# Kernel tuning notes

Measured on AMD Instinct MI355X. Metric: run time of the kernel, lower is better.

Reference implementation:

```python
import jax, jax.numpy as jnp
import numpy as np

B, S, N, D, T = 128, 128, 196, 512, 12


def setup_inputs() -> dict:
    key = jax.random.key(0)
    ks = jax.random.split(key, 20)
    nrm = lambda i, shape, s: jax.random.normal(ks[i], shape, jnp.float32) * s
    w = lambda i, shape: nrm(i, shape, 1.0 / np.sqrt(shape[-1]))
    return {
        "ctx": nrm(0, (B, S, D), 1.0),
        "q": nrm(1, (B, 2 * D), 1.0),
        "k": nrm(2, (B, D, N), 1.0),
        "mem0": nrm(3, (1, D), 0.02),
        "ctrl0": nrm(4, (1, D), 0.02),
        # ControlUnit params
        "Wp": w(5, (T, D, 2 * D)), "bp": jnp.zeros((T, D), jnp.float32),
        "Wcq": w(6, (D, 2 * D)), "bcq": jnp.zeros((D,), jnp.float32),
        "Wca": w(7, (1, D)), "bca": jnp.zeros((1,), jnp.float32),
        # ReadUnit params
        "Wrm": w(8, (D, D)), "brm": jnp.zeros((D,), jnp.float32),
        "Wrc": w(9, (D, 2 * D)), "brc": jnp.zeros((D,), jnp.float32),
        "Wra": w(10, (1, D)), "bra": jnp.zeros((1,), jnp.float32),
        # WriteUnit params
        "Wwc": w(11, (D, 2 * D)), "bwc": jnp.zeros((D,), jnp.float32),
    }


def reference(ctx, q, k, mem0, ctrl0, Wp, bp, Wcq, bcq, Wca, bca,
              Wrm, brm, Wrc, brc, Wra, bra, Wwc, bwc):
    b = q.shape[0]
    c = jnp.broadcast_to(ctrl0, (b, D))
    m = jnp.broadcast_to(mem0, (b, D))
    for t in range(T):
        # --- control unit (alpha_entmax with alpha=1.0 == softmax) ---
        p = q @ Wp[t].T + bp[t]                                # [B, D]
        cc = jnp.concatenate([c, p], axis=1) @ Wcq.T + bcq     # [B, D]
        ctx_p = cc[:, None, :] * ctx                           # [B, S, D]
        aw = jax.nn.softmax(ctx_p @ Wca.T + bca, axis=1)       # [B, S, 1]
        c = (aw * ctx).sum(axis=1)                             # [B, D]
        # --- read unit ---
        mm = (m @ Wrm.T + brm)[:, :, None]                     # [B, D, 1]
        kc = jnp.concatenate([mm * k, k], axis=1)              # [B, 2D, N]
        rc = kc.transpose(0, 2, 1) @ Wrc.T + brc               # [B, N, D]
        logit = ((rc * c[:, None, :]) @ Wra.T + bra)[..., 0]   # [B, N]
        rw = jax.nn.softmax(logit, axis=1)[:, None, :]         # [B, 1, N]
        r = (rw * k).sum(axis=2)                               # [B, D]
        # --- write unit (no self-attention / memory gate) ---
        m = jnp.concatenate([r, m], axis=1) @ Wwc.T + bwc      # [B, D]
    return m
```

## Files before the change

### kernel.cpp

```cpp
#include <hip/hip_runtime.h>
#include <hip/hip_bf16.h>
#include <cstdint>

#define D  512
#define D2 1024
#define BB 128
#define SS 128
#define NN 196
#define TT 12

typedef unsigned short u16;
typedef __attribute__((ext_vector_type(8))) short short8v;
typedef __attribute__((ext_vector_type(4))) float f32x4;

__device__ __forceinline__ float bf2f(u16 h){
  union { unsigned int u; float f; } v; v.u = ((unsigned int)h) << 16; return v.f;
}

__device__ __forceinline__ float LDX(const void* p, size_t i, int isbf){
  if (isbf) return bf2f(((const u16*)p)[i]);
  return ((const float*)p)[i];
}

__device__ __forceinline__ float4 LD4(const void* p, size_t i, int isbf){
  if (isbf){
    ushort4 w = *(const ushort4*)((const u16*)p + i);
    return make_float4(bf2f(w.x), bf2f(w.y), bf2f(w.z), bf2f(w.w));
  }
  return *(const float4*)((const float*)p + i);
}

__device__ __forceinline__ void bfsplit(float x, short &h, short &l){
  unsigned u = __float_as_uint(x);
  unsigned hu = u & 0xFFFF0000u;
  float r = x - __uint_as_float(hu);
  h = (short)(u >> 16);
  l = (short)(__float_as_uint(r) >> 16);
}

__global__ __launch_bounds__(256) void k_detect(const u16* ctx, int* flag){
  __shared__ int cnt;
  if (threadIdx.x == 0) cnt = 0;
  __syncthreads();
  int bad = 0;
  for (int i = threadIdx.x; i < 8192; i += 256){
    int e = (ctx[i] >> 7) & 0xFF;
    if (e == 0xFF || (e != 0 && (e < 90 || e > 160))) bad++;
  }
  atomicAdd(&cnt, bad);
  __syncthreads();
  if (threadIdx.x == 0) *flag = (cnt > 100) ? 0 : 1;
}

__global__ __launch_bounds__(256) void k_prep1(const void* Wcq, const void* Wca,
      const void* Wwc, const void* Wrm, const void* Wrc, const void* Wra,
      const void* bp, const void* bcq, const void* ctrl0, const void* mem0, const void* brm,
      float* W1f, float* Wwcf, float* WrmTf, float* W2f,
      float* P, float* pp2, float* ubase, float* mmb, const int* flag){
  const int isbf = *flag;
  __shared__ float lds[32][33];
  int bk = blockIdx.x, tid = threadIdx.x;
  int tx = tid & 31, ty = tid >> 5;
  if (bk >= 1216){
    int ib = bk - 1216;
    int lane = tid & 63, w = tid >> 6;
    int grp = lane >> 3, k = lane & 7;
    int isU = (ib < 16);
    int o = (isU ? ib : ib - 16)*32 + w*8 + grp;
    const void* vec = isU ? ctrl0 : mem0;
    const void* mat = isU ? Wcq : Wrm;
    int ld = isU ? D2 : D;
    float acc = 0.f;
    #pragma unroll 4
    for (int it = 0; it < 16; it++){
      int d = it*32 + k*4;
      float4 v = LD4(vec, d, isbf);
      float4 m = LD4(mat, (size_t)o*ld + d, isbf);
      acc += v.x*m.x + v.y*m.y + v.z*m.z + v.w*m.w;
    }
    acc += __shfl_xor(acc, 1, 64);
    acc += __shfl_xor(acc, 2, 64);
    acc += __shfl_xor(acc, 4, 64);
    if (k == 0){
      if (isU) ubase[o] = acc * LDX(Wca, o, isbf);
      else     mmb[o]   = acc + LDX(brm, o, isbf);
    }
    return;
  }
  if (bk >= 1152){
    int l = bk - 1152;
    for (int idx = l*256 + tid; idx < 786432; idx += 64*256){
      int j = (idx >> 7) & 511;
      pp2[idx] = LDX(bcq, j, isbf) * LDX(Wca, j, isbf);
    }
    return;
  }
  if (bk >= 1088){
    int l = bk - 1088;
    for (int idx = l*256 + tid; idx < 786432; idx += 64*256)
      P[idx] = LDX(bp, idx >> 7, isbf);
    return;
  }
  if (bk >= 1024){
    int l = bk - 1024;
    if (isbf){
      const u16* w = (const u16*)Wrc; const u16* s = (const u16*)Wra;
      for (int idx = l*256 + tid; idx < 524288; idx += 64*256)
        W2f[idx] = bf2f(w[idx]) * bf2f(s[idx >> 10]);
    } else {
      const float* w = (const float*)Wrc; const float* s = (const float*)Wra;
      for (int idx = l*256 + tid; idx < 524288; idx += 64*256)
        W2f[idx] = w[idx] * s[idx >> 10];
    }
    return;
  }
  const void* in = nullptr; const void* scale = nullptr; float* out = nullptr;
  int ld = 0, R = 0, tR = 0, tC = 0;
  if (bk < 256)      { int l = bk;       in = Wcq; ld = 1024; R = 512; out = W1f;  scale = Wca; tR = l & 15; tC = l >> 4; }
  else if (bk < 768) { int l = bk - 256; in = Wwc; ld = 1024; R = 512; out = Wwcf; tR = l & 15; tC = l >> 4; }
  else               { int l = bk - 768; in = Wrm; ld = 512;  R = 512; out = WrmTf;tR = l & 15; tC = l >> 4; }
  int r0 = tR*32, c0 = tC*32;
  #pragma unroll
  for (int kk = 0; kk < 4; kk++){
    int r = r0 + ty + kk*8;
    float v = LDX(in, (size_t)r*ld + c0 + tx, isbf);
    if (scale) v *= LDX(scale, r, isbf);
    lds[tx][ty + kk*8] = v;
  }
  __syncthreads();
  #pragma unroll
  for (int kk = 0; kk < 4; kk++){
    int oc = ty + kk*8;
    out[(size_t)(c0 + oc)*R + r0 + tx] = lds[oc][tx];
  }
}

__global__ __launch_bounds__(256) void k_pack(const void* q, u16* QF,
                                              const void* kmat, float* kT, const int* flag){
  const int isbf = *flag;
  __shared__ float lds[64][201];
  int bk = blockIdx.x, tid = threadIdx.x;
  if (bk < 128){
    u16* QH = QF;
    u16* QL = QF + 131072;
    for (int idx = bk*256 + tid; idx < 131072; idx += 128*256){
      int b = idx >> 10, x = idx & 1023;
      int o = ((x >> 3) << 10) + (b << 3) + (x & 7);
      if (isbf){
        QH[o] = ((const u16*)q)[idx];
        QL[o] = 0;
      } else {
        short h, l;
        bfsplit(((const float*)q)[idx], h, l);
        QH[o] = (u16)h;
        QL[o] = (u16)l;
      }
    }
    return;
  }
  int l = bk - 128;
  int b = l >> 3, dt = l & 7;
  int d0 = dt*64;
  int r = tid >> 2, q4 = tid & 3;
  const size_t rowbase = ((size_t)b*D + d0 + r)*NN;
  #pragma unroll
  for (int p = 0; p < 13; p++){
    int j = q4 + p*4;
    if (j < 49){
      float4 v = LD4(kmat, rowbase + 4*j, isbf);
      *(float4*)&lds[r][4*j] = v;
    }
  }
  __syncthreads();
  int n_loc = tid >> 4, f = tid & 15;
  #pragma unroll
  for (int p = 0; p < 13; p++){
    int n = p*16 + n_loc;
    if (n < NN){
      float4 v = make_float4(lds[4*f][n], lds[4*f+1][n], lds[4*f+2][n], lds[4*f+3][n]);
      *(float4*)&kT[((size_t)b*NN + n)*D + d0 + 4*f] = v;
    }
  }
}

__global__ __launch_bounds__(256) void k_Pmfma(const void* Wp, const u16* QF,
                                               float* P, const int* flag){
  const int isbf = *flag;
  const u16* QH = QF;
  const u16* QL = QF + 131072;
  int bk = blockIdx.x;
  int mt = bk >> 2, kc = bk & 3;
  int m0 = mt * 32;
  int tid = threadIdx.x;
  int ln = tid & 63, w = tid >> 6;
  int msub = w >> 1, nh = w & 1;
  int row  = m0 + msub*16 + (ln & 15);
  int koff = ln >> 4;
  f32x4 acc[4];
  #pragma unroll
  for (int i = 0; i < 4; i++) acc[i] = (f32x4){0.f, 0.f, 0.f, 0.f};

  for (int ks = 0; ks < 8; ks++){
    int k0 = kc*256 + ks*32;
    short8v ah, al;
    if (isbf){
      const u16* wr = (const u16*)Wp + (size_t)row*D2 + k0 + koff*8;
      ah = *(const short8v*)wr;
    } else {
      const float* wr = (const float*)Wp + (size_t)row*D2 + k0 + koff*8;
      float4 f0 = *(const float4*)wr;
      float4 f1 = *(const float4*)(wr + 4);
      float fs[8] = {f0.x, f0.y, f0.z, f0.w, f1.x, f1.y, f1.z, f1.w};
      #pragma unroll
      for (int j = 0; j < 8; j++){
        short h, l;
        bfsplit(fs[j], h, l);
        ah[j] = h; al[j] = l;
      }
    }
    int qrow = ((k0 >> 3) + koff) << 10;
    #pragma unroll
    for (int nt = 0; nt < 4; nt++){
      int col = (nh*4 + nt)*16 + (ln & 15);
      short8v bh = *(const short8v*)(QH + qrow + (col << 3));
      acc[nt] = __builtin_amdgcn_mfma_f32_16x16x32_bf16(ah, bh, acc[nt], 0, 0, 0);
      if (!isbf){
        short8v bl = *(const short8v*)(QL + qrow + (col << 3));
        acc[nt] = __builtin_amdgcn_mfma_f32_16x16x32_bf16(ah, bl, acc[nt], 0, 0, 0);
        acc[nt] = __builtin_amdgcn_mfma_f32_16x16x32_bf16(al, bh, acc[nt], 0, 0, 0);
      }
    }
  }
  int orow = m0 + msub*16 + (ln >> 4)*4;
  #pragma unroll
  for (int nt = 0; nt < 4; nt++){
    int b = (nh*4 + nt)*16 + (ln & 15);
    #pragma unroll
    for (int r = 0; r < 4; r++)
      atomicAdd(&P[(size_t)(orow + r)*BB + b], acc[nt][r]);
  }
}

__global__ __launch_bounds__(512) void k_pp2(const float* P, const void* Wcq,
                                             const void* Wca, float* pp2, const int* flag){
  const int isbf = *flag;
  int bk = blockIdx.x;
  int t = bk >> 6; int r = bk & 63; int jt = r >> 1; int kc = r & 1;
  int tid = threadIdx.x;
  int b = tid & 127;
  int ih = __builtin_amdgcn_readfirstlane(tid >> 7);
  int j0 = jt*16 + ih*4;
  float acc[4] = {0.f, 0.f, 0.f, 0.f};
  int e0k = kc*256;
  if (isbf){
    const u16* w = (const u16*)Wcq;
    for (int e = e0k; e < e0k + 256; e += 8){
      float a[8];
      #pragma unroll
      for (int u = 0; u < 8; u++) a[u] = P[(size_t)(t*D + e + u)*BB + b];
      #pragma unroll
      for (int kk = 0; kk < 4; kk++){
        ushort4 w0 = *(const ushort4*)(w + (size_t)(j0+kk)*D2 + D + e);
        ushort4 w1 = *(const ushort4*)(w + (size_t)(j0+kk)*D2 + D + e + 4);
        acc[kk] += a[0]*bf2f(w0.x) + a[1]*bf2f(w0.y) + a[2]*bf2f(w0.z) + a[3]*bf2f(w0.w)
                 + a[4]*bf2f(w1.x) + a[5]*bf2f(w1.y) + a[6]*bf2f(w1.z) + a[7]*bf2f(w1.w);
      }
    }
  } else {
    const float* w = (const float*)Wcq;
    for (int e = e0k; e < e0k + 256; e += 8){
      float a[8];
      #pragma unroll
      for (int u = 0; u < 8; u++) a[u] = P[(size_t)(t*D + e + u)*BB + b];
      #pragma unroll
      for (int kk = 0; kk < 4; kk++){
        float4 w0 = *(const float4*)(w + (size_t)(j0+kk)*D2 + D + e);
        float4 w1 = *(const float4*)(w + (size_t)(j0+kk)*D2 + D + e + 4);
        acc[kk] += a[0]*w0.x + a[1]*w0.y + a[2]*w0.z + a[3]*w0.w
                 + a[4]*w1.x + a[5]*w1.y + a[6]*w1.z + a[7]*w1.w;
      }
    }
  }
  #pragma unroll
  for (int kk = 0; kk < 4; kk++)
    atomicAdd(&pp2[(size_t)(t*D + j0 + kk)*BB + b], acc[kk] * LDX(Wca, j0 + kk, isbf));
}

__global__ __launch_bounds__(256) void k_initB(const float* ubase, const void* mem0,
                                               const float* pp2,
                                               float* u0, float* act0, const int* flag){
  const int isbf = *flag;
  for (int idx = blockIdx.x*256 + threadIdx.x; idx < 2*D*BB; idx += 64*256){
    if (idx < D*BB) u0[idx] = ubase[idx >> 7] + pp2[idx];
    else          { int x = idx - D*BB; act0[D*BB + x] = LDX(mem0, x >> 7, isbf); }
  }
}

__global__ __launch_bounds__(512) void k_K1(const void* ctx, const float* u_cur,
                                            float* gbuf, const float* pbuf, const float* kT,
                                            float* r_out, int t, const int* flag){
  __shared__ float sm[1024];
  int bk = blockIdx.x, tid = threadIdx.x;
  const int isbf = *flag;
  if (bk < 512){
    if (t == 0) return;
    float* lg   = sm;
    float* red  = sm + 256;
    float* psum = sm + 512;
    int b = bk & 127, qc = bk >> 7;
    if (tid < 256){
      float s;
      if (tid < NN){
        s = 0.f;
        #pragma unroll
        for (int c = 0; c < 8; c++)
          s += pbuf[((size_t)c*BB + b)*256 + tid];
      } else s = -INFINITY;
      lg[tid] = s; red[tid] = s;
    }
    __syncthreads();
    for (int off = 128; off; off >>= 1){ if (tid < off) red[tid] = fmaxf(red[tid], red[tid+off]); __syncthreads(); }
    float M = red[0];
    __syncthreads();
    if (tid < 256){ float e = (tid < NN) ? __expf(lg[tid] - M) : 0.f; lg[tid] = e; red[tid] = e; }
    __syncthreads();
    for (int off = 128; off; off >>= 1){ if (tid < off) red[tid] += red[tid+off]; __syncthreads(); }
    float inv = 1.f / red[0];
    int ng = tid >> 7, dl = tid & 127;
    const float* kTb = kT + ((size_t)b*NN + ng*49)*D + qc*128 + dl;
    float acc = 0.f;
    for (int j = 0; j < 49; j++)
      acc += lg[ng*49 + j] * kTb[(size_t)j*D];
    psum[ng*128 + dl] = acc;
    __syncthreads();
    if (tid < 128)
      r_out[(size_t)(qc*128 + tid)*BB + b] =
        (psum[tid] + psum[128 + tid] + psum[256 + tid] + psum[384 + tid]) * inv;
    return;
  }
  if (t >= TT) return;
  int l = bk - 512;
  int b = l & 127, sc = l >> 7;
  float* us = sm;
  us[tid] = u_cur[(size_t)tid*BB + b];
  __syncthreads();
  int lane = tid & 63, wv = tid >> 6;
  float ur[8];
  #pragma unroll
  for (int j = 0; j < 8; j++) ur[j] = us[lane*8 + j];
  #pragma unroll
  for (int rr = 0; rr < 4; rr++){
    int s = sc*32 + wv*4 + rr;
    size_t base = ((size_t)(b*SS + s))*D + lane*8;
    float4 c0 = LD4(ctx, base, isbf);
    float4 c1 = LD4(ctx, base + 4, isbf);
    float dot = ur[0]*c0.x + ur[1]*c0.y + ur[2]*c0.z + ur[3]*c0.w
              + ur[4]*c1.x + ur[5]*c1.y + ur[6]*c1.z + ur[7]*c1.w;
    #pragma unroll
    for (int off = 32; off; off >>= 1) dot += __shfl_down(dot, off, 64);
    if (lane == 0) gbuf[b*SS + s] = dot;
  }
}

__global__ __launch_bounds__(512) void k_K2(const void* ctx, const float* gbuf, float* cbuf,
                                            const float* act_prev, float* act_cur,
                                            float* u_nxt, const float* pp2_next,
                                            const float* Wwcf, int t, const int* flag){
  __shared__ float sm[768];
  int bk = blockIdx.x, tid = threadIdx.x;
  const int isbf = *flag;
  if (bk < 512){
    float* lg   = sm;
    float* red  = sm + 128;
    float* psum = sm + 256;
    int b = bk & 127, qc = bk >> 7;
    if (tid < 128){ float v = gbuf[b*SS + tid]; lg[tid] = v; red[tid] = v; }
    __syncthreads();
    for (int off = 64; off; off >>= 1){ if (tid < off) red[tid] = fmaxf(red[tid], red[tid+off]); __syncthreads(); }
    float M = red[0];
    __syncthreads();
    if (tid < 128){ float e = __expf(lg[tid] - M); lg[tid] = e; red[tid] = e; }
    __syncthreads();
    for (int off = 64; off; off >>= 1){ if (tid < off) red[tid] += red[tid+off]; __syncthreads(); }
    float inv = 1.f / red[0];
    int sg = tid >> 7, dl = tid & 127;
    int d = qc*128 + dl;
    float acc = 0.f;
    for (int j = 0; j < 32; j++){
      int s = sg*32 + j;
      acc += lg[s] * LDX(ctx, ((size_t)(b*SS + s))*D + d, isbf);
    }
    psum[sg*128 + dl] = acc;
    __syncthreads();
    if (tid < 128)
      cbuf[(size_t)(qc*128 + tid)*BB + b] =
        (psum[tid] + psum[128 + tid] + psum[256 + tid] + psum[384 + tid]) * inv;
    return;
  }
  int b = tid & 127;
  int ih = __builtin_amdgcn_readfirstlane(tid >> 7);
  if (bk < 1024){
    if (t == 0) return;
    int l = bk - 512;
    int it = l >> 3, kc = l & 7;
    int ih0 = ih & 1, ih1 = ih >> 1;
    int i0 = it*8 + ih0*4;
    int e0 = kc*128 + ih1*64;
    float acc[4] = {0.f,0.f,0.f,0.f};
    for (int e = e0; e < e0 + 64; e += 8){
      float av[8];
      #pragma unroll
      for (int u = 0; u < 8; u++) av[u] = act_prev[(size_t)(e+u)*BB + b];
      #pragma unroll
      for (int u = 0; u < 8; u++){
        float4 w0 = *(const float4*)(Wwcf + (size_t)(e+u)*D + i0);
        acc[0]+=av[u]*w0.x; acc[1]+=av[u]*w0.y; acc[2]+=av[u]*w0.z; acc[3]+=av[u]*w0.w;
      }
    }
    #pragma unroll
    for (int kk = 0; kk < 4; kk++)
      atomicAdd(&act_cur[(size_t)(D + i0 + kk)*BB + b], acc[kk]);
  } else {
    if (t >= TT-1) return;
    int l = bk - 1024;
    for (int x = l*512 + tid; x < D*BB; x += 32*512) u_nxt[x] = pp2_next[x];
  }
}

__global__ __launch_bounds__(512) void k_KC1(const void* kmat, const float* cbuf,
                                             const float* act_cur, const float* W2f,
                                             const float* WrmTf, const void* brm,
                                             const float* mmb, float* pbuf,
                                             const float* W1f, float* u_nxt,
                                             float* act_nxt, const void* bwc,
                                             int t, const int* flag){
  __shared__ float cb[512];
  __shared__ float mv[512];
  __shared__ float wv2[256];
  __shared__ float mmv[128];
  __shared__ float u2[128];
  int bk = blockIdx.x, tid = threadIdx.x;
  const int isbf = *flag;
  if (bk < 512){
    int b = bk & 127, ch2 = bk >> 7;
    int d0 = ch2*128;
    cb[tid] = cbuf[(size_t)tid*BB + b];
    if (t > 0) mv[tid] = act_cur[(size_t)(D + tid)*BB + b];
    __syncthreads();
    if (tid < 256){
      int e = (tid < 128) ? (d0 + tid) : (D + d0 + (tid - 128));
      float c0=0.f,c1=0.f,c2=0.f,c3=0.f,c4=0.f,c5=0.f,c6=0.f,c7=0.f;
      for (int j = 0; j < 512; j += 8){
        c0 += cb[j  ]*W2f[(size_t)(j  )*D2 + e];
        c1 += cb[j+1]*W2f[(size_t)(j+1)*D2 + e];
        c2 += cb[j+2]*W2f[(size_t)(j+2)*D2 + e];
        c3 += cb[j+3]*W2f[(size_t)(j+3)*D2 + e];
        c4 += cb[j+4]*W2f[(size_t)(j+4)*D2 + e];
        c5 += cb[j+5]*W2f[(size_t)(j+5)*D2 + e];
        c6 += cb[j+6]*W2f[(size_t)(j+6)*D2 + e];
        c7 += cb[j+7]*W2f[(size_t)(j+7)*D2 + e];
      }
      wv2[tid] = (((c0+c1)+(c2+c3)) + ((c4+c5)+(c6+c7)));
    } else if (tid < 384){
      int tm = tid - 256;
      int d = d0 + tm;
      if (t == 0){
        mmv[tm] = mmb[d];
      } else {
        float c0=0.f,c1=0.f,c2=0.f,c3=0.f,c4=0.f,c5=0.f,c6=0.f,c7=0.f;
        for (int j = 0; j < 512; j += 8){
          c0 += mv[j  ]*WrmTf[(size_t)(j  )*D + d];
          c1 += mv[j+1]*WrmTf[(size_t)(j+1)*D + d];
          c2 += mv[j+2]*WrmTf[(size_t)(j+2)*D + d];
          c3 += mv[j+3]*WrmTf[(size_t)(j+3)*D + d];
          c4 += mv[j+4]*WrmTf[(size_t)(j+4)*D + d];
          c5 += mv[j+5]*WrmTf[(size_t)(j+5)*D + d];
          c6 += mv[j+6]*WrmTf[(size_t)(j+6)*D + d];
          c7 += mv[j+7]*WrmTf[(size_t)(j+7)*D + d];
        }
        mmv[tm] = LDX(brm, d, isbf) + (((c0+c1)+(c2+c3)) + ((c4+c5)+(c6+c7)));
      }
    }
    __syncthreads();
    if (tid < 128) u2[tid] = wv2[tid]*mmv[tid] + wv2[128 + tid];
    __syncthreads();
    int half = tid >> 8;
    int n = tid & 255;
    int dd0 = half*64;
    float part = 0.f;
    if (n < NN){
      float c[8];
      #pragma unroll
      for (int u = 0; u < 8; u++) c[u] = 0.f;
      if (isbf){
        const u16* kb = (const u16*)kmat + (size_t)b*D*NN + (size_t)(d0+dd0)*NN + n;
        for (int dd = 0; dd < 64; dd += 8){
          #pragma unroll
          for (int u = 0; u < 8; u++) c[u] += u2[dd0+dd+u]*bf2f(kb[(size_t)(dd+u)*NN]);
        }
      } else {
        const float* kb = (const float*)kmat + (size_t)b*D*NN + (size_t)(d0+dd0)*NN + n;
        for (int dd = 0; dd < 64; dd += 8){
          #pragma unroll
          for (int u = 0; u < 8; u++) c[u] += u2[dd0+dd+u]*kb[(size_t)(dd+u)*NN];
        }
      }
      part = (((c[0]+c[1]) + (c[2]+c[3])) + ((c[4]+c[5]) + (c[6]+c[7])));
    }
    int chunk = ch2*2 + half;
    pbuf[((size_t)chunk*BB + b)*256 + n] = part;
    return;
  }
  int b = tid & 127;
  int ih = __builtin_amdgcn_readfirstlane(tid >> 7);
  if (bk < 768){
    if (t >= TT-1) return;
    int l = bk - 512;
    int jt = l >> 1, kc = l & 1;
    int j = jt*4 + ih;
    float c0 = 0.f, c1 = 0.f, c2 = 0.f, c3 = 0.f, c4 = 0.f, c5 = 0.f, c6 = 0.f, c7 = 0.f;
    int e0 = kc*256;
    for (int e = e0; e < e0 + 256; e += 8){
      c0 += cbuf[(e  )*BB + b] * W1f[(size_t)(e  )*D + j];
      c1 += cbuf[(e+1)*BB + b] * W1f[(size_t)(e+1)*D + j];
      c2 += cbuf[(e+2)*BB + b] * W1f[(size_t)(e+2)*D + j];
      c3 += cbuf[(e+3)*BB + b] * W1f[(size_t)(e+3)*D + j];
      c4 += cbuf[(e+4)*BB + b] * W1f[(size_t)(e+4)*D + j];
      c5 += cbuf[(e+5)*BB + b] * W1f[(size_t)(e+5)*D + j];
      c6 += cbuf[(e+6)*BB + b] * W1f[(size_t)(e+6)*D + j];
      c7 += cbuf[(e+7)*BB + b] * W1f[(size_t)(e+7)*D + j];
    }
    float acc = (((c0+c1)+(c2+c3)) + ((c4+c5)+(c6+c7)));
    atomicAdd(&u_nxt[(size_t)j*BB + b], acc);
  } else {
    int l = bk - 768;
    for (int x = l*512 + tid; x < D*BB; x += 32*512)
      act_nxt[D*BB + x] = LDX(bwc, x >> 7, isbf);
  }
}

__global__ __launch_bounds__(512) void k_moutA(const float* act_fin, const float* Wwcf,
                                               float* act_out){
  int bk = blockIdx.x, tid = threadIdx.x;
  int b = tid & 127;
  int ih = __builtin_amdgcn_readfirstlane(tid >> 7);
  int it = bk >> 3, kc = bk & 7;
  int ih0 = ih & 1, ih1 = ih >> 1;
  int i0 = it*8 + ih0*4;
  int e0 = kc*128 + ih1*64;
  float acc[4] = {0.f,0.f,0.f,0.f};
  for (int e = e0; e < e0 + 64; e += 8){
    float av[8];
    #pragma unroll
    for (int u = 0; u < 8; u++) av[u] = act_fin[(size_t)(e+u)*BB + b];
    #pragma unroll
    for (int u = 0; u < 8; u++){
      float4 w0 = *(const float4*)(Wwcf + (size_t)(e+u)*D + i0);
      acc[0]+=av[u]*w0.x; acc[1]+=av[u]*w0.y; acc[2]+=av[u]*w0.z; acc[3]+=av[u]*w0.w;
    }
  }
  #pragma unroll
  for (int kk = 0; kk < 4; kk++)
    atomicAdd(&act_out[(size_t)(D + i0 + kk)*BB + b], acc[kk]);
}

__global__ __launch_bounds__(256) void k_outT(const float* act_fin, void* out, const int* flag){
  const int isbf = *flag;
  __shared__ float lds[32][33];
  int bk = blockIdx.x;
  int it = bk >> 2, bt = bk & 3;
  int tx = threadIdx.x & 31, ty = threadIdx.x >> 5;
  #pragma unroll
  for (int kk = 0; kk < 4; kk++){
    int i = it*32 + ty + kk*8;
    lds[tx][ty + kk*8] = act_fin[(size_t)(D + i)*BB + bt*32 + tx];
  }
  __syncthreads();
  if (isbf){
    __hip_bfloat16* o = (__hip_bfloat16*)out;
    #pragma unroll
    for (int kk = 0; kk < 4; kk++){
      int bb = bt*32 + ty + kk*8;
      o[(size_t)bb*D + it*32 + tx] = __float2bfloat16(lds[ty + kk*8][tx]);
    }
  } else {
    float* o = (float*)out;
    #pragma unroll
    for (int kk = 0; kk < 4; kk++){
      int bb = bt*32 + ty + kk*8;
      o[(size_t)bb*D + it*32 + tx] = lds[ty + kk*8][tx];
    }
  }
}

extern "C" void kernel_launch(void* const* d_in, const int* in_sizes, int n_in,
                              void* d_out, int out_size, void* d_ws, size_t ws_size,
                              hipStream_t stream){
  const void* ctx  = d_in[0];
  const void* q    = d_in[1];
  const void* kmat = d_in[2];
  const void* mem0 = d_in[3];
  const void* ctrl0= d_in[4];
  const void* Wp   = d_in[5];
  const void* bp   = d_in[6];
  const void* Wcq  = d_in[7];
  const void* bcq  = d_in[8];
  const void* Wca  = d_in[9];
  const void* Wrm  = d_in[11];
  const void* brm  = d_in[12];
  const void* Wrc  = d_in[13];
  const void* Wra  = d_in[15];
  const void* Wwc  = d_in[17];
  const void* bwc  = d_in[18];

  float* W      = (float*)d_ws;
  float* qT     = W;
  float* P      = W + 131072;
  float* pp2    = W + 917504;
  float* W1f    = W + 1703936;
  float* W2f    = W + 1966080;
  float* Wwcf   = W + 2490368;
  float* WrmTf  = W + 3014656;
  float* cbuf   = W + 3276800;
  float* actb   = W + 3538944;
  float* ubuf   = W + 3801088;
  int*   flag   = (int*)(W + 3932160);
  float* ubase  = W + 3932224;
  float* mmb    = W + 3932736;
  float* gbuf   = W + 3933248;
  float* pbuf   = P;
  float* kT     = W + 4194304;

  hipLaunchKernelGGL(k_detect, dim3(1), dim3(256), 0, stream, (const u16*)ctx, flag);
  hipLaunchKernelGGL(k_prep1, dim3(1248), dim3(256), 0, stream,
                     Wcq, Wca, Wwc, Wrm, Wrc, Wra, bp, bcq, ctrl0, mem0, brm,
                     W1f, Wwcf, WrmTf, W2f, P, pp2, ubase, mmb, flag);
  hipLaunchKernelGGL(k_pack, dim3(1152), dim3(256), 0, stream,
                     q, (u16*)qT, kmat, kT, flag);
  hipLaunchKernelGGL(k_Pmfma, dim3(768), dim3(256), 0, stream, Wp, (const u16*)qT, P, flag);
  hipLaunchKernelGGL(k_pp2,  dim3(768), dim3(512), 0, stream, P, Wcq, Wca, pp2, flag);
  hipLaunchKernelGGL(k_initB, dim3(64), dim3(256), 0, stream,
                     ubase, mem0, pp2, ubuf, actb, flag);

  for (int t = 0; t < TT; t++){
    int cur = t & 1, nxt = 1 - cur;
    float* act_cur  = actb + cur*131072;
    float* act_prev = actb + nxt*131072;
    hipLaunchKernelGGL(k_K1, dim3(1024), dim3(512), 0, stream,
                       ctx, ubuf + cur*65536, gbuf, pbuf, kT,
                       act_prev, t, flag);
    hipLaunchKernelGGL(k_K2, dim3(1056), dim3(512), 0, stream,
                       ctx, gbuf, cbuf, act_prev, act_cur,
                       ubuf + nxt*65536,
                       pp2 + ((t+1 < TT) ? (t+1)*65536 : 0), Wwcf, t, flag);
    hipLaunchKernelGGL(k_KC1, dim3(800), dim3(512), 0, stream,
                       kmat, cbuf, act_cur, W2f, WrmTf, brm, mmb, pbuf,
                       W1f, ubuf + nxt*65536,
                       actb + nxt*131072, bwc, t, flag);
  }
  hipLaunchKernelGGL(k_K1, dim3(512), dim3(512), 0, stream,
                     ctx, ubuf, gbuf, pbuf, kT,
                     actb + 131072, TT, flag);
  hipLaunchKernelGGL(k_moutA, dim3(512), dim3(512), 0, stream,
                     actb + 131072, Wwcf, actb);
  hipLaunchKernelGGL(k_outT, dim3(64), dim3(256), 0, stream, actb, d_out, flag);
}
```

Before: 1.010 ms.

## Fuse recurrent loop into one persistent cooperative kernel with grid syncs

The 12-step loop of three kernel launches per step is replaced by a single cooperative kernel of 256 blocks. Each block loops over virtual block indices, and the former kernel boundaries become grid.sync barriers. The kernel bodies are factored into shared device functions, and the old multi-launch path stays as a fallback if the cooperative launch fails. This removes per-launch overhead and inter-kernel gaps. In exchange it cuts the number of resident blocks per phase, serializes work within each block, and pays the cost of grid-wide barriers.

New measurement: 2.663 ms. 164% more time.

```diff
diff --git a/kernel.cpp b/kernel.cpp
--- a/kernel.cpp
+++ b/kernel.cpp
@@ -1,6 +1,9 @@
 #include <hip/hip_runtime.h>
 #include <hip/hip_bf16.h>
+#include <hip/hip_cooperative_groups.h>
 #include <cstdint>
+
+namespace cg = cooperative_groups;
 
 #define D  512
 #define D2 1024
@@ -296,51 +299,46 @@
   }
 }
 
-__global__ __launch_bounds__(512) void k_K1(const void* ctx, const float* u_cur,
-                                            float* gbuf, const float* pbuf, const float* kT,
-                                            float* r_out, int t, const int* flag){
-  __shared__ float sm[1024];
-  int bk = blockIdx.x, tid = threadIdx.x;
-  const int isbf = *flag;
-  if (bk < 512){
-    if (t == 0) return;
-    float* lg   = sm;
-    float* red  = sm + 256;
-    float* psum = sm + 512;
-    int b = bk & 127, qc = bk >> 7;
-    if (tid < 256){
-      float s;
-      if (tid < NN){
-        s = 0.f;
-        #pragma unroll
-        for (int c = 0; c < 8; c++)
-          s += pbuf[((size_t)c*BB + b)*256 + tid];
-      } else s = -INFINITY;
-      lg[tid] = s; red[tid] = s;
-    }
-    __syncthreads();
-    for (int off = 128; off; off >>= 1){ if (tid < off) red[tid] = fmaxf(red[tid], red[tid+off]); __syncthreads(); }
-    float M = red[0];
-    __syncthreads();
-    if (tid < 256){ float e = (tid < NN) ? __expf(lg[tid] - M) : 0.f; lg[tid] = e; red[tid] = e; }
-    __syncthreads();
-    for (int off = 128; off; off >>= 1){ if (tid < off) red[tid] += red[tid+off]; __syncthreads(); }
-    float inv = 1.f / red[0];
-    int ng = tid >> 7, dl = tid & 127;
-    const float* kTb = kT + ((size_t)b*NN + ng*49)*D + qc*128 + dl;
-    float acc = 0.f;
-    for (int j = 0; j < 49; j++)
-      acc += lg[ng*49 + j] * kTb[(size_t)j*D];
-    psum[ng*128 + dl] = acc;
-    __syncthreads();
-    if (tid < 128)
-      r_out[(size_t)(qc*128 + tid)*BB + b] =
-        (psum[tid] + psum[128 + tid] + psum[256 + tid] + psum[384 + tid]) * inv;
-    return;
-  }
-  if (t >= TT) return;
-  int l = bk - 512;
-  int b = l & 127, sc = l >> 7;
+__device__ __forceinline__ void body_kfinish(const float* pbuf, const float* kT,
+                                             float* r_out, int vb, int tid, float* sm){
+  float* lg   = sm;
+  float* red  = sm + 256;
+  float* psum = sm + 512;
+  int b = vb & 127, qc = vb >> 7;
+  if (tid < 256){
+    float s;
+    if (tid < NN){
+      s = 0.f;
+      #pragma unroll
+      for (int c = 0; c < 8; c++)
+        s += pbuf[((size_t)c*BB + b)*256 + tid];
+    } else s = -INFINITY;
+    lg[tid] = s; red[tid] = s;
+  }
+  __syncthreads();
+  for (int off = 128; off; off >>= 1){ if (tid < off) red[tid] = fmaxf(red[tid], red[tid+off]); __syncthreads(); }
+  float M = red[0];
+  __syncthreads();
+  if (tid < 256){ float e = (tid < NN) ? __expf(lg[tid] - M) : 0.f; lg[tid] = e; red[tid] = e; }
+  __syncthreads();
+  for (int off = 128; off; off >>= 1){ if (tid < off) red[tid] += red[tid+off]; __syncthreads(); }
+  float inv = 1.f / red[0];
+  int ng = tid >> 7, dl = tid & 127;
+  const float* kTb = kT + ((size_t)b*NN + ng*49)*D + qc*128 + dl;
+  float acc = 0.f;
+  for (int j = 0; j < 49; j++)
+    acc += lg[ng*49 + j] * kTb[(size_t)j*D];
+  psum[ng*128 + dl] = acc;
+  __syncthreads();
+  if (tid < 128)
+    r_out[(size_t)(qc*128 + tid)*BB + b] =
+      (psum[tid] + psum[128 + tid] + psum[256 + tid] + psum[384 + tid]) * inv;
+}
+
+__device__ __forceinline__ void body_ctxlogit(const void* ctx, const float* u_cur,
+                                              float* gbuf, int vb, int tid, int isbf,
+                                              float* sm){
+  int b = vb & 127, sc = vb >> 7;
   float* us = sm;
   us[tid] = u_cur[(size_t)tid*BB + b];
   __syncthreads();
@@ -362,64 +360,249 @@
   }
 }
 
+__device__ __forceinline__ void body_ctxfin(const void* ctx, const float* gbuf, float* cbuf,
+                                            int vb, int tid, int isbf, float* sm){
+  float* lg   = sm;
+  float* red  = sm + 128;
+  float* psum = sm + 256;
+  int b = vb & 127, qc = vb >> 7;
+  if (tid < 128){ float v = gbuf[b*SS + tid]; lg[tid] = v; red[tid] = v; }
+  __syncthreads();
+  for (int off = 64; off; off >>= 1){ if (tid < off) red[tid] = fmaxf(red[tid], red[tid+off]); __syncthreads(); }
+  float M = red[0];
+  __syncthreads();
+  if (tid < 128){ float e = __expf(lg[tid] - M); lg[tid] = e; red[tid] = e; }
+  __syncthreads();
+  for (int off = 64; off; off >>= 1){ if (tid < off) red[tid] += red[tid+off]; __syncthreads(); }
+  float inv = 1.f / red[0];
+  int sg = tid >> 7, dl = tid & 127;
+  int d = qc*128 + dl;
+  float acc = 0.f;
+  for (int j = 0; j < 32; j++){
+    int s = sg*32 + j;
+    acc += lg[s] * LDX(ctx, ((size_t)(b*SS + s))*D + d, isbf);
+  }
+  psum[sg*128 + dl] = acc;
+  __syncthreads();
+  if (tid < 128)
+    cbuf[(size_t)(qc*128 + tid)*BB + b] =
+      (psum[tid] + psum[128 + tid] + psum[256 + tid] + psum[384 + tid]) * inv;
+}
+
+__device__ __forceinline__ void body_mgemv(const float* act_prev, const float* Wwcf,
+                                           float* act_cur, int vb, int tid){
+  int b = tid & 127;
+  int ih = __builtin_amdgcn_readfirstlane(tid >> 7);
+  int it = vb >> 3, kc = vb & 7;
+  int ih0 = ih & 1, ih1 = ih >> 1;
+  int i0 = it*8 + ih0*4;
+  int e0 = kc*128 + ih1*64;
+  float acc[4] = {0.f,0.f,0.f,0.f};
+  for (int e = e0; e < e0 + 64; e += 8){
+    float av[8];
+    #pragma unroll
+    for (int u = 0; u < 8; u++) av[u] = act_prev[(size_t)(e+u)*BB + b];
+    #pragma unroll
+    for (int u = 0; u < 8; u++){
+      float4 w0 = *(const float4*)(Wwcf + (size_t)(e+u)*D + i0);
+      acc[0]+=av[u]*w0.x; acc[1]+=av[u]*w0.y; acc[2]+=av[u]*w0.z; acc[3]+=av[u]*w0.w;
+    }
+  }
+  #pragma unroll
+  for (int kk = 0; kk < 4; kk++)
+    atomicAdd(&act_cur[(size_t)(D + i0 + kk)*BB + b], acc[kk]);
+}
+
+__device__ __forceinline__ void body_fused(const void* kmat, const float* cbuf,
+                                           const float* act_cur, const float* W2f,
+                                           const float* WrmTf, const void* brm,
+                                           const float* mmb, float* pbuf,
+                                           int vb, int tid, int t, int isbf,
+                                           float* cb, float* mvs, float* wv2,
+                                           float* mmv, float* u2s){
+  int b = vb & 127, ch2 = vb >> 7;
+  int d0 = ch2*128;
+  cb[tid] = cbuf[(size_t)tid*BB + b];
+  if (t > 0) mvs[tid] = act_cur[(size_t)(D + tid)*BB + b];
+  __syncthreads();
+  if (tid < 256){
+    int e = (tid < 128) ? (d0 + tid) : (D + d0 + (tid - 128));
+    float c0=0.f,c1=0.f,c2=0.f,c3=0.f,c4=0.f,c5=0.f,c6=0.f,c7=0.f;
+    for (int j = 0; j < 512; j += 8){
+      c0 += cb[j  ]*W2f[(size_t)(j  )*D2 + e];
+      c1 += cb[j+1]*W2f[(size_t)(j+1)*D2 + e];
+      c2 += cb[j+2]*W2f[(size_t)(j+2)*D2 + e];
+      c3 += cb[j+3]*W2f[(size_t)(j+3)*D2 + e];
+      c4 += cb[j+4]*W2f[(size_t)(j+4)*D2 + e];
+      c5 += cb[j+5]*W2f[(size_t)(j+5)*D2 + e];
+      c6 += cb[j+6]*W2f[(size_t)(j+6)*D2 + e];
+      c7 += cb[j+7]*W2f[(size_t)(j+7)*D2 + e];
+    }
+    wv2[tid] = (((c0+c1)+(c2+c3)) + ((c4+c5)+(c6+c7)));
+  } else if (tid < 384){
+    int tm = tid - 256;
+    int d = d0 + tm;
+    if (t == 0){
+      mmv[tm] = mmb[d];
+    } else {
+      float c0=0.f,c1=0.f,c2=0.f,c3=0.f,c4=0.f,c5=0.f,c6=0.f,c7=0.f;
+      for (int j = 0; j < 512; j += 8){
+        c0 += mvs[j  ]*WrmTf[(size_t)(j  )*D + d];
+        c1 += mvs[j+1]*WrmTf[(size_t)(j+1)*D + d];
+        c2 += mvs[j+2]*WrmTf[(size_t)(j+2)*D + d];
+        c3 += mvs[j+3]*WrmTf[(size_t)(j+3)*D + d];
+        c4 += mvs[j+4]*WrmTf[(size_t)(j+4)*D + d];
+        c5 += mvs[j+5]*WrmTf[(size_t)(j+5)*D + d];
+        c6 += mvs[j+6]*WrmTf[(size_t)(j+6)*D + d];
+        c7 += mvs[j+7]*WrmTf[(size_t)(j+7)*D + d];
+      }
+      mmv[tm] = LDX(brm, d, isbf) + (((c0+c1)+(c2+c3)) + ((c4+c5)+(c6+c7)));
+    }
+  }
+  __syncthreads();
+  if (tid < 128) u2s[tid] = wv2[tid]*mmv[tid] + wv2[128 + tid];
+  __syncthreads();
+  int half = tid >> 8;
+  int n = tid & 255;
+  int dd0 = half*64;
+  float part = 0.f;
+  if (n < NN){
+    float c[8];
+    #pragma unroll
+    for (int u = 0; u < 8; u++) c[u] = 0.f;
+    if (isbf){
+      const u16* kb = (const u16*)kmat + (size_t)b*D*NN + (size_t)(d0+dd0)*NN + n;
+      for (int dd = 0; dd < 64; dd += 8){
+        #pragma unroll
+        for (int u = 0; u < 8; u++) c[u] += u2s[dd0+dd+u]*bf2f(kb[(size_t)(dd+u)*NN]);
+      }
+    } else {
+      const float* kb = (const float*)kmat + (size_t)b*D*NN + (size_t)(d0+dd0)*NN + n;
+      for (int dd = 0; dd < 64; dd += 8){
+        #pragma unroll
+        for (int u = 0; u < 8; u++) c[u] += u2s[dd0+dd+u]*kb[(size_t)(dd+u)*NN];
+      }
+    }
+    part = (((c[0]+c[1]) + (c[2]+c[3])) + ((c[4]+c[5]) + (c[6]+c[7])));
+  }
+  int chunk = ch2*2 + half;
+  pbuf[((size_t)chunk*BB + b)*256 + n] = part;
+}
+
+__device__ __forceinline__ void body_ugemv(const float* cbuf, const float* W1f,
+                                           float* u_nxt, int vb, int tid){
+  int b = tid & 127;
+  int ih = __builtin_amdgcn_readfirstlane(tid >> 7);
+  int jt = vb >> 1, kc = vb & 1;
+  int j = jt*4 + ih;
+  float c0 = 0.f, c1 = 0.f, c2 = 0.f, c3 = 0.f, c4 = 0.f, c5 = 0.f, c6 = 0.f, c7 = 0.f;
+  int e0 = kc*256;
+  for (int e = e0; e < e0 + 256; e += 8){
+    c0 += cbuf[(e  )*BB + b] * W1f[(size_t)(e  )*D + j];
+    c1 += cbuf[(e+1)*BB + b] * W1f[(size_t)(e+1)*D + j];
+    c2 += cbuf[(e+2)*BB + b] * W1f[(size_t)(e+2)*D + j];
+    c3 += cbuf[(e+3)*BB + b] * W1f[(size_t)(e+3)*D + j];
+    c4 += cbuf[(e+4)*BB + b] * W1f[(size_t)(e+4)*D + j];
+    c5 += cbuf[(e+5)*BB + b] * W1f[(size_t)(e+5)*D + j];
+    c6 += cbuf[(e+6)*BB + b] * W1f[(size_t)(e+6)*D + j];
+    c7 += cbuf[(e+7)*BB + b] * W1f[(size_t)(e+7)*D + j];
+  }
+  float acc = (((c0+c1)+(c2+c3)) + ((c4+c5)+(c6+c7)));
+  atomicAdd(&u_nxt[(size_t)j*BB + b], acc);
+}
+
+__global__ __launch_bounds__(512, 2) void k_loop(
+    const void* ctx, const void* kmat, const float* kT,
+    const float* W1f, const float* W2f, const float* WrmTf, const float* Wwcf,
+    const void* brm, const void* bwc, const float* mmb, const float* pp2,
+    float* gbuf, float* pbuf, float* cbuf, float* actb, float* ubuf,
+    const int* flag){
+  cg::grid_group grid = cg::this_grid();
+  const int isbf = *flag;
+  const int bid = blockIdx.x, tid = threadIdx.x;
+  __shared__ float sm[1024];
+  __shared__ float cb[512];
+  __shared__ float mvs[512];
+  __shared__ float wv2[256];
+  __shared__ float mmv[128];
+  __shared__ float u2s[128];
+
+  for (int t = 0; t < TT; t++){
+    const int cur = t & 1, nxt = 1 - cur;
+    float* act_cur  = actb + cur*131072;
+    float* act_prev = actb + nxt*131072;
+    const float* u_cur = ubuf + cur*65536;
+    float* u_nxt = ubuf + nxt*65536;
+    const float* pp2_next = pp2 + ((t+1 < TT) ? (t+1)*65536 : 0);
+
+    #pragma unroll 1
+    for (int vb = bid; vb < 512; vb += 256){
+      if (t > 0) body_kfinish(pbuf, kT, act_prev, vb, tid, sm);
+      __syncthreads();
+      body_ctxlogit(ctx, u_cur, gbuf, vb, tid, isbf, sm);
+      __syncthreads();
+    }
+    grid.sync();
+
+    #pragma unroll 1
+    for (int vb = bid; vb < 512; vb += 256){
+      body_ctxfin(ctx, gbuf, cbuf, vb, tid, isbf, sm);
+      __syncthreads();
+    }
+    if (t > 0){
+      #pragma unroll 1
+      for (int vb = bid; vb < 512; vb += 256)
+        body_mgemv(act_prev, Wwcf, act_cur, vb, tid);
+    }
+    if (bid < 32 && t < TT-1){
+      for (int x = bid*512 + tid; x < D*BB; x += 32*512) u_nxt[x] = pp2_next[x];
+    }
+    grid.sync();
+
+    #pragma unroll 1
+    for (int vb = bid; vb < 512; vb += 256){
+      body_fused(kmat, cbuf, act_cur, W2f, WrmTf, brm, mmb, pbuf,
+                 vb, tid, t, isbf, cb, mvs, wv2, mmv, u2s);
+      __syncthreads();
+    }
+    if (t < TT-1)
+      body_ugemv(cbuf, W1f, u_nxt, bid, tid);
+    if (bid < 32){
+      for (int x = bid*512 + tid; x < D*BB; x += 32*512)
+        act_prev[D*BB + x] = LDX(bwc, x >> 7, isbf);
+    }
+    grid.sync();
+  }
+}
+
+__global__ __launch_bounds__(512) void k_K1(const void* ctx, const float* u_cur,
+                                            float* gbuf, const float* pbuf, const float* kT,
+                                            float* r_out, int t, const int* flag){
+  __shared__ float sm[1024];
+  int bk = blockIdx.x, tid = threadIdx.x;
+  const int isbf = *flag;
+  if (bk < 512){
+    if (t == 0) return;
+    body_kfinish(pbuf, kT, r_out, bk, tid, sm);
+    return;
+  }
+  if (t >= TT) return;
+  body_ctxlogit(ctx, u_cur, gbuf, bk - 512, tid, isbf, sm);
+}
+
 __global__ __launch_bounds__(512) void k_K2(const void* ctx, const float* gbuf, float* cbuf,
                                             const float* act_prev, float* act_cur,
                                             float* u_nxt, const float* pp2_next,
                                             const float* Wwcf, int t, const int* flag){
   __shared__ float sm[768];
   int bk = blockIdx.x, tid = threadIdx.x;
-  const int isbf = *flag;
   if (bk < 512){
-    float* lg   = sm;
-    float* red  = sm + 128;
-    float* psum = sm + 256;
-    int b = bk & 127, qc = bk >> 7;
-    if (tid < 128){ float v = gbuf[b*SS + tid]; lg[tid] = v; red[tid] = v; }
-    __syncthreads();
-    for (int off = 64; off; off >>= 1){ if (tid < off) red[tid] = fmaxf(red[tid], red[tid+off]); __syncthreads(); }
-    float M = red[0];
-    __syncthreads();
-    if (tid < 128){ float e = __expf(lg[tid] - M); lg[tid] = e; red[tid] = e; }
-    __syncthreads();
-    for (int off = 64; off; off >>= 1){ if (tid < off) red[tid] += red[tid+off]; __syncthreads(); }
-    float inv = 1.f / red[0];
-    int sg = tid >> 7, dl = tid & 127;
-    int d = qc*128 + dl;
-    float acc = 0.f;
-    for (int j = 0; j < 32; j++){
-      int s = sg*32 + j;
-      acc += lg[s] * LDX(ctx, ((size_t)(b*SS + s))*D + d, isbf);
-    }
-    psum[sg*128 + dl] = acc;
-    __syncthreads();
-    if (tid < 128)
-      cbuf[(size_t)(qc*128 + tid)*BB + b] =
-        (psum[tid] + psum[128 + tid] + psum[256 + tid] + psum[384 + tid]) * inv;
+    body_ctxfin(ctx, gbuf, cbuf, bk, tid, *flag, sm);
     return;
   }
-  int b = tid & 127;
-  int ih = __builtin_amdgcn_readfirstlane(tid >> 7);
   if (bk < 1024){
     if (t == 0) return;
-    int l = bk - 512;
-    int it = l >> 3, kc = l & 7;
-    int ih0 = ih & 1, ih1 = ih >> 1;
-    int i0 = it*8 + ih0*4;
-    int e0 = kc*128 + ih1*64;
-    float acc[4] = {0.f,0.f,0.f,0.f};
-    for (int e = e0; e < e0 + 64; e += 8){
-      float av[8];
-      #pragma unroll
-      for (int u = 0; u < 8; u++) av[u] = act_prev[(size_t)(e+u)*BB + b];
-      #pragma unroll
-      for (int u = 0; u < 8; u++){
-        float4 w0 = *(const float4*)(Wwcf + (size_t)(e+u)*D + i0);
-        acc[0]+=av[u]*w0.x; acc[1]+=av[u]*w0.y; acc[2]+=av[u]*w0.z; acc[3]+=av[u]*w0.w;
-      }
-    }
-    #pragma unroll
-    for (int kk = 0; kk < 4; kk++)
-      atomicAdd(&act_cur[(size_t)(D + i0 + kk)*BB + b], acc[kk]);
+    body_mgemv(act_prev, Wwcf, act_cur, bk - 512, tid);
   } else {
     if (t >= TT-1) return;
     int l = bk - 1024;
@@ -435,108 +618,31 @@
                                              float* act_nxt, const void* bwc,
                                              int t, const int* flag){
   __shared__ float cb[512];
-  __shared__ float mv[512];
+  __shared__ float mvs[512];
   __shared__ float wv2[256];
   __shared__ float mmv[128];
-  __shared__ float u2[128];
+  __shared__ float u2s[128];
   int bk = blockIdx.x, tid = threadIdx.x;
   const int isbf = *flag;
   if (bk < 512){
-    int b = bk & 127, ch2 = bk >> 7;
-    int d0 = ch2*128;
-    cb[tid] = cbuf[(size_t)tid*BB + b];
-    if (t > 0) mv[tid] = act_cur[(size_t)(D + tid)*BB + b];
-    __syncthreads();
-    if (tid < 256){
-      int e = (tid < 128) ? (d0 + tid) : (D + d0 + (tid - 128));
-      float c0=0.f,c1=0.f,c2=0.f,c3=0.f,c4=0.f,c5=0.f,c6=0.f,c7=0.f;
-      for (int j = 0; j < 512; j += 8){
-        c0 += cb[j  ]*W2f[(size_t)(j  )*D2 + e];
-        c1 += cb[j+1]*W2f[(size_t)(j+1)*D2 + e];
-        c2 += cb[j+2]*W2f[(size_t)(j+2)*D2 + e];
-        c3 += cb[j+3]*W2f[(size_t)(j+3)*D2 + e];
-        c4 += cb[j+4]*W2f[(size_t)(j+4)*D2 + e];
-        c5 += cb[j+5]*W2f[(size_t)(j+5)*D2 + e];
-        c6 += cb[j+6]*W2f[(size_t)(j+6)*D2 + e];
-        c7 += cb[j+7]*W2f[(size_t)(j+7)*D2 + e];
-      }
-      wv2[tid] = (((c0+c1)+(c2+c3)) + ((c4+c5)+(c6+c7)));
-    } else if (tid < 384){
-      int tm = tid - 256;
-      int d = d0 + tm;
-      if (t == 0){
-        mmv[tm] = mmb[d];
-      } else {
-        float c0=0.f,c1=0.f,c2=0.f,c3=0.f,c4=0.f,c5=0.f,c6=0.f,c7=0.f;
-        for (int j = 0; j < 512; j += 8){
-          c0 += mv[j  ]*WrmTf[(size_t)(j  )*D + d];
-          c1 += mv[j+1]*WrmTf[(size_t)(j+1)*D + d];
-          c2 += mv[j+2]*WrmTf[(size_t)(j+2)*D + d];
-          c3 += mv[j+3]*WrmTf[(size_t)(j+3)*D + d];
-          c4 += mv[j+4]*WrmTf[(size_t)(j+4)*D + d];
-          c5 += mv[j+5]*WrmTf[(size_t)(j+5)*D + d];
-          c6 += mv[j+6]*WrmTf[(size_t)(j+6)*D + d];
-          c7 += mv[j+7]*WrmTf[(size_t)(j+7)*D + d];
-        }
-        mmv[tm] = LDX(brm, d, isbf) + (((c0+c1)+(c2+c3)) + ((c4+c5)+(c6+c7)));
-      }
-    }
-    __syncthreads();
-    if (tid < 128) u2[tid] = wv2[tid]*mmv[tid] + wv2[128 + tid];
-    __syncthreads();
-    int half = tid >> 8;
-    int n = tid & 255;
-    int dd0 = half*64;
-    float part = 0.f;
-    if (n < NN){
-      float c[8];
-      #pragma unroll
-      for (int u = 0; u < 8; u++) c[u] = 0.f;
-      if (isbf){
-        const u16* kb = (const u16*)kmat + (size_t)b*D*NN + (size_t)(d0+dd0)*NN + n;
-        for (int dd = 0; dd < 64; dd += 8){
-          #pragma unroll
-          for (int u = 0; u < 8; u++) c[u] += u2[dd0+dd+u]*bf2f(kb[(size_t)(dd+u)*NN]);
-        }
-      } else {
-        const float* kb = (const float*)kmat + (size_t)b*D*NN + (size_t)(d0+dd0)*NN + n;
-        for (int dd = 0; dd < 64; dd += 8){
-          #pragma unroll
-          for (int u = 0; u < 8; u++) c[u] += u2[dd0+dd+u]*kb[(size_t)(dd+u)*NN];
-        }
-      }
-      part = (((c[0]+c[1]) + (c[2]+c[3])) + ((c[4]+c[5]) + (c[6]+c[7])));
-    }
-    int chunk = ch2*2 + half;
-    pbuf[((size_t)chunk*BB + b)*256 + n] = part;
+    body_fused(kmat, cbuf, act_cur, W2f, WrmTf, brm, mmb, pbuf,
+               bk, tid, t, isbf, cb, mvs, wv2, mmv, u2s);
     return;
   }
-  int b = tid & 127;
-  int ih = __builtin_amdgcn_readfirstlane(tid >> 7);
   if (bk < 768){
     if (t >= TT-1) return;
-    int l = bk - 512;
-    int jt = l >> 1, kc = l & 1;
-    int j = jt*4 + ih;
-    float c0 = 0.f, c1 = 0.f, c2 = 0.f, c3 = 0.f, c4 = 0.f, c5 = 0.f, c6 = 0.f, c7 = 0.f;
-    int e0 = kc*256;
-    for (int e = e0; e < e0 + 256; e += 8){
-      c0 += cbuf[(e  )*BB + b] * W1f[(size_t)(e  )*D + j];
-      c1 += cbuf[(e+1)*BB + b] * W1f[(size_t)(e+1)*D + j];
-      c2 += cbuf[(e+2)*BB + b] * W1f[(size_t)(e+2)*D + j];
-      c3 += cbuf[(e+3)*BB + b] * W1f[(size_t)(e+3)*D + j];
-      c4 += cbuf[(e+4)*BB + b] * W1f[(size_t)(e+4)*D + j];
-      c5 += cbuf[(e+5)*BB + b] * W1f[(size_t)(e+5)*D + j];
-      c6 += cbuf[(e+6)*BB + b] * W1f[(size_t)(e+6)*D + j];
-      c7 += cbuf[(e+7)*BB + b] * W1f[(size_t)(e+7)*D + j];
-    }
-    float acc = (((c0+c1)+(c2+c3)) + ((c4+c5)+(c6+c7)));
-    atomicAdd(&u_nxt[(size_t)j*BB + b], acc);
+    body_ugemv(cbuf, W1f, u_nxt, bk - 512, tid);
   } else {
     int l = bk - 768;
     for (int x = l*512 + tid; x < D*BB; x += 32*512)
       act_nxt[D*BB + x] = LDX(bwc, x >> 7, isbf);
   }
+}
+
+__global__ __launch_bounds__(512) void k_K1fin(const float* pbuf, const float* kT,
+                                               float* r_out){
+  __shared__ float sm[1024];
+  body_kfinish(pbuf, kT, r_out, blockIdx.x, threadIdx.x, sm);
 }
 
 __global__ __launch_bounds__(512) void k_moutA(const float* act_fin, const float* Wwcf,
@@ -642,25 +748,46 @@
   hipLaunchKernelGGL(k_initB, dim3(64), dim3(256), 0, stream,
                      ubase, mem0, pp2, ubuf, actb, flag);
 
-  for (int t = 0; t < TT; t++){
-    int cur = t & 1, nxt = 1 - cur;
-    float* act_cur  = actb + cur*131072;
-    float* act_prev = actb + nxt*131072;
-    hipLaunchKernelGGL(k_K1, dim3(1024), dim3(512), 0, stream,
-                       ctx, ubuf + cur*65536, gbuf, pbuf, kT,
-                       act_prev, t, flag);
-    hipLaunchKernelGGL(k_K2, dim3(1056), dim3(512), 0, stream,
-                       ctx, gbuf, cbuf, act_prev, act_cur,
-                       ubuf + nxt*65536,
-                       pp2 + ((t+1 < TT) ? (t+1)*65536 : 0), Wwcf, t, flag);
-    hipLaunchKernelGGL(k_KC1, dim3(800), dim3(512), 0, stream,
-                       kmat, cbuf, act_cur, W2f, WrmTf, brm, mmb, pbuf,
-                       W1f, ubuf + nxt*65536,
-                       actb + nxt*131072, bwc, t, flag);
-  }
-  hipLaunchKernelGGL(k_K1, dim3(512), dim3(512), 0, stream,
-                     ctx, ubuf, gbuf, pbuf, kT,
-                     actb + 131072, TT, flag);
+  hipError_t cerr;
+  {
+    const void* ctx_a = ctx;  const void* kmat_a = kmat;
+    const float* kT_a = kT;   const float* W1f_a = W1f;  const float* W2f_a = W2f;
+    const float* WrmTf_a = WrmTf; const float* Wwcf_a = Wwcf;
+    const void* brm_a = brm;  const void* bwc_a = bwc;
+    const float* mmb_a = mmb; const float* pp2_a = pp2;
+    float* gbuf_a = gbuf; float* pbuf_a = pbuf; float* cbuf_a = cbuf;
+    float* actb_a = actb; float* ubuf_a = ubuf;
+    const int* flag_a = flag;
+    void* kargs[] = {
+      (void*)&ctx_a, (void*)&kmat_a, (void*)&kT_a, (void*)&W1f_a, (void*)&W2f_a,
+      (void*)&WrmTf_a, (void*)&Wwcf_a, (void*)&brm_a, (void*)&bwc_a, (void*)&mmb_a,
+      (void*)&pp2_a, (void*)&gbuf_a, (void*)&pbuf_a, (void*)&cbuf_a,
+      (void*)&actb_a, (void*)&ubuf_a, (void*)&flag_a
+    };
+    cerr = hipLaunchCooperativeKernel((const void*)k_loop, dim3(256), dim3(512),
+                                      kargs, 0, stream);
+  }
+  if (cerr != hipSuccess){
+    for (int t = 0; t < TT; t++){
+      int cur = t & 1, nxt = 1 - cur;
+      float* act_cur  = actb + cur*131072;
+      float* act_prev = actb + nxt*131072;
+      hipLaunchKernelGGL(k_K1, dim3(1024), dim3(512), 0, stream,
+                         ctx, ubuf + cur*65536, gbuf, pbuf, kT,
+                         act_prev, t, flag);
+      hipLaunchKernelGGL(k_K2, dim3(1056), dim3(512), 0, stream,
+                         ctx, gbuf, cbuf, act_prev, act_cur,
+                         ubuf + nxt*65536,
+                         pp2 + ((t+1 < TT) ? (t+1)*65536 : 0), Wwcf, t, flag);
+      hipLaunchKernelGGL(k_KC1, dim3(800), dim3(512), 0, stream,
+                         kmat, cbuf, act_cur, W2f, WrmTf, brm, mmb, pbuf,
+                         W1f, ubuf + nxt*65536,
+                         actb + nxt*131072, bwc, t, flag);
+    }
+  }
+
+  hipLaunchKernelGGL(k_K1fin, dim3(512), dim3(512), 0, stream,
+                     pbuf, kT, actb + 131072);
   hipLaunchKernelGGL(k_moutA, dim3(512), dim3(512), 0, stream,
                      actb + 131072, Wwcf, actb);
   hipLaunchKernelGGL(k_outT, dim3(64), dim3(256), 0, stream, actb, d_out, flag);
```
